# Optimization experiments

Measured on AMD Instinct MI355X. Metric: run time of the kernel, lower is better.

The kernel has to match this reference:

```python
import jax, jax.numpy as jnp
import numpy as np

H = 8  # nhead
EPS = 1e-5


def _ln(x, g, b):
    mu = x.mean(-1, keepdims=True)
    var = ((x - mu) ** 2).mean(-1, keepdims=True)
    return (x - mu) / jnp.sqrt(var + EPS) * g + b


def _mha(q_in, kv_in, w_qkv, b_qkv, w_o, b_o, mask):
    # PyTorch nn.MultiheadAttention with packed in_proj: rows [Wq; Wk; Wv], y = x @ W.T + b
    d = q_in.shape[-1]
    hd = d // H
    wq, wk, wv = jnp.split(w_qkv, 3, axis=0)
    bq, bk, bv = jnp.split(b_qkv, 3)
    B, Lq = q_in.shape[0], q_in.shape[1]
    Lk = kv_in.shape[1]
    q = (q_in @ wq.T + bq).reshape(B, Lq, H, hd).transpose(0, 2, 1, 3)
    k = (kv_in @ wk.T + bk).reshape(B, Lk, H, hd).transpose(0, 2, 1, 3)
    v = (kv_in @ wv.T + bv).reshape(B, Lk, H, hd).transpose(0, 2, 1, 3)
    s = jnp.einsum('bhqd,bhkd->bhqk', q, k) * np.float32(1.0 / np.sqrt(hd))
    if mask is not None:
        s = s + mask  # additive causal mask, (Lq, Lk) broadcast
    a = jax.nn.softmax(s, axis=-1)
    o = jnp.einsum('bhqk,bhkd->bhqd', a, v).transpose(0, 2, 1, 3).reshape(B, Lq, d)
    return o @ w_o.T + b_o


def _forward(z, target_ids, tok_emb, pos_emb, lp_w, lp_b, lp_ln_g, lp_ln_b,
             sa_qkv_w, sa_qkv_b, sa_out_w, sa_out_b,
             ca_qkv_w, ca_qkv_b, ca_out_w, ca_out_b,
             ln1_g, ln1_b, ln2_g, ln2_b, ln3_g, ln3_b,
             ff1_w, ff1_b, ff2_w, ff2_b, op_w, op_b):
    B, L = target_ids.shape
    # latent_proj: Linear -> GELU (exact) -> LayerNorm; (B, 1, d) memory
    mem = jax.nn.gelu(z @ lp_w.T + lp_b, approximate=False)
    mem = _ln(mem, lp_ln_g, lp_ln_b)[:, None, :]
    # token + positional embedding
    x = tok_emb[target_ids] + pos_emb[jnp.arange(L)][None, :, :]
    # causal additive mask (upper triangle = -inf)
    causal = jnp.where(jnp.tril(jnp.ones((L, L), dtype=bool)), 0.0, -1e9).astype(x.dtype)
    n_layers = sa_qkv_w.shape[0]
    for i in range(n_layers):  # post-norm TransformerDecoderLayer (norm_first=False)
        x = _ln(x + _mha(x, x, sa_qkv_w[i], sa_qkv_b[i], sa_out_w[i], sa_out_b[i], causal), ln1_g[i], ln1_b[i])
        x = _ln(x + _mha(x, mem, ca_qkv_w[i], ca_qkv_b[i], ca_out_w[i], ca_out_b[i], None), ln2_g[i], ln2_b[i])
        ff = jax.nn.relu(x @ ff1_w[i].T + ff1_b[i]) @ ff2_w[i].T + ff2_b[i]
        x = _ln(x + ff, ln3_g[i], ln3_b[i])
    return x @ op_w.T + op_b  # (B, L, vocab)


def setup_inputs() -> dict:
    B, L, D, LAT, V, NL = 32, 128, 512, 256, 50257, 4
    DF = 4 * D
    key = jax.random.key(0)
    ks = jax.random.split(key, 20)
    s = 0.02
    n = lambda k, shp: jax.random.normal(k, shp, dtype=jnp.float32) * s
    return {
        'z': jax.random.normal(ks[0], (B, LAT), dtype=jnp.float32),
        'target_ids': jax.random.randint(ks[1], (B, L), 0, V),
        'tok_emb': n(ks[2], (V, D)),
        'pos_emb': n(ks[3], (L, D)),
        'lp_w': n(ks[4], (D, LAT)), 'lp_b': jnp.zeros((D,)),
        'lp_ln_g': jnp.ones((D,)), 'lp_ln_b': jnp.zeros((D,)),
        'sa_qkv_w': n(ks[5], (NL, 3 * D, D)), 'sa_qkv_b': jnp.zeros((NL, 3 * D)),
        'sa_out_w': n(ks[6], (NL, D, D)), 'sa_out_b': jnp.zeros((NL, D)),
        'ca_qkv_w': n(ks[7], (NL, 3 * D, D)), 'ca_qkv_b': jnp.zeros((NL, 3 * D)),
        'ca_out_w': n(ks[8], (NL, D, D)), 'ca_out_b': jnp.zeros((NL, D)),
        'ln1_g': jnp.ones((NL, D)), 'ln1_b': jnp.zeros((NL, D)),
        'ln2_g': jnp.ones((NL, D)), 'ln2_b': jnp.zeros((NL, D)),
        'ln3_g': jnp.ones((NL, D)), 'ln3_b': jnp.zeros((NL, D)),
        'ff1_w': n(ks[9], (NL, DF, D)), 'ff1_b': jnp.zeros((NL, DF)),
        'ff2_w': n(ks[10], (NL, D, DF)), 'ff2_b': jnp.zeros((NL, D)),
        'op_w': n(ks[11], (V, D)), 'op_b': jnp.zeros((V,)),
    }


def reference(z, target_ids, tok_emb, pos_emb, lp_w, lp_b, lp_ln_g, lp_ln_b,
              sa_qkv_w, sa_qkv_b, sa_out_w, sa_out_b,
              ca_qkv_w, ca_qkv_b, ca_out_w, ca_out_b,
              ln1_g, ln1_b, ln2_g, ln2_b, ln3_g, ln3_b,
              ff1_w, ff1_b, ff2_w, ff2_b, op_w, op_b):
    return _forward(z, target_ids, tok_emb, pos_emb, lp_w, lp_b, lp_ln_g, lp_ln_b,
                    sa_qkv_w, sa_qkv_b, sa_out_w, sa_out_b,
                    ca_qkv_w, ca_qkv_b, ca_out_w, ca_out_b,
                    ln1_g, ln1_b, ln2_g, ln2_b, ln3_g, ln3_b,
                    ff1_w, ff1_b, ff2_w, ff2_b, op_w, op_b)
```

## Files before the change

### kernel.cpp

```cpp
#include <hip/hip_runtime.h>
#include <math.h>

typedef __attribute__((ext_vector_type(8))) short short8;
typedef __attribute__((ext_vector_type(4))) float f32x4;
typedef __attribute__((ext_vector_type(4))) float f4;
typedef __attribute__((ext_vector_type(4))) unsigned short us4;
typedef unsigned short u16;

#define Bn 32
#define Ln 128
#define Dn 512
#define LATn 256
#define Vn 50257
#define VPAD 50304
#define DFn 2048
#define Hn 8
#define HDn 64

#define GLD(src, dst) __builtin_amdgcn_global_load_lds( \
    (const __attribute__((address_space(1))) unsigned int*)(src), \
    (__attribute__((address_space(3))) unsigned int*)(dst), 16, 0, 0)

__device__ __forceinline__ u16 f2bf(float f) {
  union { float f; unsigned u; } v; v.f = f;
  unsigned r = 0x7FFFu + ((v.u >> 16) & 1u);
  return (u16)((v.u + r) >> 16);
}
__device__ __forceinline__ float bf2f(u16 u) {
  union { unsigned u; float f; } v; v.u = ((unsigned)u) << 16;
  return v.f;
}

__global__ __launch_bounds__(256)
void k_cvt_all(const float* __restrict__ s0, const float* __restrict__ s1,
               const float* __restrict__ s2, const float* __restrict__ s3,
               const float* __restrict__ s4, us4* __restrict__ dst) {
  const int C0 = 786432;
  const int C1 = 1048576;
  const int C2 = 2097152;
  const int C3 = 3145728;
  const int C4 = 9584640;
  const int OPN4 = 6432896;
  int i = blockIdx.x * blockDim.x + threadIdx.x;
  int stride = gridDim.x * blockDim.x;
  for (; i < C4; i += stride) {
    const f4* src; int off; bool valid = true;
    if (i < C0)      { src = (const f4*)s0; off = i; }
    else if (i < C1) { src = (const f4*)s1; off = i - C0; }
    else if (i < C2) { src = (const f4*)s2; off = i - C1; }
    else if (i < C3) { src = (const f4*)s3; off = i - C2; }
    else             { src = (const f4*)s4; off = i - C3; valid = off < OPN4; }
    us4 o;
    if (valid) {
      f4 v = src[off];
      o[0] = f2bf(v[0]); o[1] = f2bf(v[1]); o[2] = f2bf(v[2]); o[3] = f2bf(v[3]);
    } else { o[0] = 0; o[1] = 0; o[2] = 0; o[3] = 0; }
    dst[i] = o;
  }
}

__global__ __launch_bounds__(256)
void k_latent_mem(const float* __restrict__ z, const float* __restrict__ lp_w,
                  const float* __restrict__ lp_b, const float* __restrict__ g,
                  const float* __restrict__ be, float* __restrict__ mem) {
  __shared__ float zs[LATn];
  __shared__ float red[16];
  int b = blockIdx.x, t = threadIdx.x;
  zs[t] = z[b * LATn + t];
  __syncthreads();
  float h[2];
  #pragma unroll
  for (int j = 0; j < 2; j++) {
    int oj = t + j * 256;
    const float* w = lp_w + (size_t)oj * LATn;
    float s0 = 0, s1 = 0, s2 = 0, s3 = 0;
    for (int k = 0; k < LATn; k += 4) {
      s0 += zs[k] * w[k]; s1 += zs[k+1] * w[k+1];
      s2 += zs[k+2] * w[k+2]; s3 += zs[k+3] * w[k+3];
    }
    float x = s0 + s1 + s2 + s3 + lp_b[oj];
    h[j] = 0.5f * x * (1.0f + erff(x * 0.70710678118654752f));
  }
  float sum = h[0] + h[1], sq = h[0]*h[0] + h[1]*h[1];
  for (int off = 32; off; off >>= 1) {
    sum += __shfl_down(sum, off, 64);
    sq  += __shfl_down(sq,  off, 64);
  }
  int lane = t & 63, wid = t >> 6;
  if (!lane) { red[wid] = sum; red[8 + wid] = sq; }
  __syncthreads();
  float ts = red[0] + red[1] + red[2] + red[3];
  float tq = red[8] + red[9] + red[10] + red[11];
  float mu = ts * (1.0f / Dn);
  float var = tq * (1.0f / Dn) - mu * mu;
  float rstd = rsqrtf(fmaxf(var, 0.0f) + 1e-5f);
  #pragma unroll
  for (int j = 0; j < 2; j++) {
    int oj = t + j * 256;
    mem[b * Dn + oj] = (h[j] - mu) * rstd * g[oj] + be[oj];
  }
}

__global__ __launch_bounds__(256)
void k_ca(const float* __restrict__ mem, const float* __restrict__ ca_qkv_w,
          const float* __restrict__ ca_qkv_b, const float* __restrict__ ca_out_w,
          const float* __restrict__ ca_out_b, float* __restrict__ ca_add) {
  int blk = blockIdx.x;
  int i = blk >> 5, b = blk & 31, t = threadIdx.x;
  __shared__ float ms[Dn];
  __shared__ float vs[Dn];
  ms[t] = mem[b * Dn + t];
  ms[t + 256] = mem[b * Dn + t + 256];
  __syncthreads();
  const float* wv = ca_qkv_w + ((size_t)i * 1536 + 1024) * Dn;
  const float* bv = ca_qkv_b + i * 1536 + 1024;
  for (int j = t; j < Dn; j += 256) {
    const float* w = wv + (size_t)j * Dn;
    float s0 = 0, s1 = 0, s2 = 0, s3 = 0;
    for (int k = 0; k < Dn; k += 4) {
      s0 += ms[k]*w[k]; s1 += ms[k+1]*w[k+1]; s2 += ms[k+2]*w[k+2]; s3 += ms[k+3]*w[k+3];
    }
    vs[j] = s0 + s1 + s2 + s3 + bv[j];
  }
  __syncthreads();
  const float* wo = ca_out_w + (size_t)i * Dn * Dn;
  const float* bo = ca_out_b + i * Dn;
  for (int j = t; j < Dn; j += 256) {
    const float* w = wo + (size_t)j * Dn;
    float s0 = 0, s1 = 0, s2 = 0, s3 = 0;
    for (int k = 0; k < Dn; k += 4) {
      s0 += vs[k]*w[k]; s1 += vs[k+1]*w[k+1]; s2 += vs[k+2]*w[k+2]; s3 += vs[k+3]*w[k+3];
    }
    ca_add[((size_t)i * Bn + b) * Dn + j] = s0 + s1 + s2 + s3 + bo[j];
  }
}

__global__ __launch_bounds__(128)
void k_embed(const int* __restrict__ ids, const float* __restrict__ tok,
             const float* __restrict__ pos, float* __restrict__ X,
             u16* __restrict__ Xb) {
  int r = blockIdx.x;
  int l = r & (Ln - 1);
  int id = ids[r];
  int c = threadIdx.x * 4;
  f4 te = *(const f4*)&tok[(size_t)id * Dn + c];
  f4 pe = *(const f4*)&pos[(size_t)l * Dn + c];
  f4 v = te + pe;
  *(f4*)&X[(size_t)r * Dn + c] = v;
  us4 o = { f2bf(v[0]), f2bf(v[1]), f2bf(v[2]), f2bf(v[3]) };
  *(us4*)&Xb[(size_t)r * Dn + c] = o;
}

__global__ __launch_bounds__(128)
void k_add_ln(float* __restrict__ X, u16* __restrict__ Xb,
              const u16* __restrict__ Y, const float* __restrict__ g,
              const float* __restrict__ be) {
  int r = blockIdx.x, t = threadIdx.x;
  int c = t * 4;
  f4 x = *(const f4*)&X[(size_t)r * Dn + c];
  us4 yb = *(const us4*)&Y[(size_t)r * Dn + c];
  f4 v;
  v[0] = x[0] + bf2f(yb[0]); v[1] = x[1] + bf2f(yb[1]);
  v[2] = x[2] + bf2f(yb[2]); v[3] = x[3] + bf2f(yb[3]);
  float sum = v[0] + v[1] + v[2] + v[3];
  float sq = v[0]*v[0] + v[1]*v[1] + v[2]*v[2] + v[3]*v[3];
  for (int off = 32; off; off >>= 1) {
    sum += __shfl_down(sum, off, 64);
    sq  += __shfl_down(sq,  off, 64);
  }
  __shared__ float red[4];
  int lane = t & 63, w = t >> 6;
  if (!lane) { red[w] = sum; red[2 + w] = sq; }
  __syncthreads();
  sum = red[0] + red[1]; sq = red[2] + red[3];
  float mu = sum * (1.0f / Dn);
  float var = sq * (1.0f / Dn) - mu * mu;
  float rstd = rsqrtf(fmaxf(var, 0.0f) + 1e-5f);
  f4 gg = *(const f4*)&g[c];
  f4 bb = *(const f4*)&be[c];
  f4 o = (v - mu) * rstd * gg + bb;
  *(f4*)&X[(size_t)r * Dn + c] = o;
  us4 ob = { f2bf(o[0]), f2bf(o[1]), f2bf(o[2]), f2bf(o[3]) };
  *(us4*)&Xb[(size_t)r * Dn + c] = ob;
}

__global__ __launch_bounds__(128)
void k_add_ln12(float* __restrict__ X, u16* __restrict__ Xb,
                const u16* __restrict__ Y, const float* __restrict__ CA,
                const float* __restrict__ g1, const float* __restrict__ b1,
                const float* __restrict__ g2, const float* __restrict__ b2) {
  int r = blockIdx.x, t = threadIdx.x;
  int c = t * 4;
  __shared__ float red[8];
  int lane = t & 63, w = t >> 6;
  f4 x = *(const f4*)&X[(size_t)r * Dn + c];
  us4 yb = *(const us4*)&Y[(size_t)r * Dn + c];
  f4 v;
  v[0] = x[0] + bf2f(yb[0]); v[1] = x[1] + bf2f(yb[1]);
  v[2] = x[2] + bf2f(yb[2]); v[3] = x[3] + bf2f(yb[3]);
  float sum = v[0] + v[1] + v[2] + v[3];
  float sq = v[0]*v[0] + v[1]*v[1] + v[2]*v[2] + v[3]*v[3];
  for (int off = 32; off; off >>= 1) {
    sum += __shfl_down(sum, off, 64);
    sq  += __shfl_down(sq,  off, 64);
  }
  if (!lane) { red[w] = sum; red[2 + w] = sq; }
  __syncthreads();
  sum = red[0] + red[1]; sq = red[2] + red[3];
  float mu = sum * (1.0f / Dn);
  float var = sq * (1.0f / Dn) - mu * mu;
  float rstd = rsqrtf(fmaxf(var, 0.0f) + 1e-5f);
  f4 g1v = *(const f4*)&g1[c];
  f4 b1v = *(const f4*)&b1[c];
  f4 o1 = (v - mu) * rstd * g1v + b1v;
  f4 ca = *(const f4*)&CA[(size_t)(r >> 7) * Dn + c];
  f4 v2 = o1 + ca;
  float sum2 = v2[0] + v2[1] + v2[2] + v2[3];
  float sq2 = v2[0]*v2[0] + v2[1]*v2[1] + v2[2]*v2[2] + v2[3]*v2[3];
  for (int off = 32; off; off >>= 1) {
    sum2 += __shfl_down(sum2, off, 64);
    sq2  += __shfl_down(sq2,  off, 64);
  }
  if (!lane) { red[4 + w] = sum2; red[6 + w] = sq2; }
  __syncthreads();
  sum2 = red[4] + red[5]; sq2 = red[6] + red[7];
  float mu2 = sum2 * (1.0f / Dn);
  float var2 = sq2 * (1.0f / Dn) - mu2 * mu2;
  float rstd2 = rsqrtf(fmaxf(var2, 0.0f) + 1e-5f);
  f4 g2v = *(const f4*)&g2[c];
  f4 b2v = *(const f4*)&b2[c];
  f4 o2 = (v2 - mu2) * rstd2 * g2v + b2v;
  *(f4*)&X[(size_t)r * Dn + c] = o2;
  us4 ob = { f2bf(o2[0]), f2bf(o2[1]), f2bf(o2[2]), f2bf(o2[3]) };
  *(us4*)&Xb[(size_t)r * Dn + c] = ob;
}

__global__ __launch_bounds__(256, 1)
void k_attn_m(const u16* __restrict__ QKV, u16* __restrict__ Ob) {
  constexpr int QS = 0;
  constexpr int KS = 9216;
  constexpr int SFB = 36864;
  constexpr int VTB = 36864 + 66048;
  constexpr int MXB = VTB + 17408;
  constexpr int LXB = MXB + 1024;
  __shared__ __align__(16) char smem[LXB + 1024];
  u16* U = (u16*)smem;
  float* Sf = (float*)(smem + SFB);
  u16* Vt = (u16*)(smem + VTB);
  float* Mx = (float*)(smem + MXB);
  float* Lx = (float*)(smem + LXB);

  int bh = blockIdx.x, b = bh >> 3, h = bh & 7;
  int tid = threadIdx.x, lane = tid & 63, wid = tid >> 6;
  int r = tid & 127, half = tid >> 7;

  {
    const u16* qk = QKV + (size_t)(b * 128 + r) * 1536 + (half ? 512 : 0) + h * 64;
    u16* dst = U + (half ? KS : QS) + r * 72;
    #pragma unroll
    for (int i = 0; i < 64; i += 8)
      *(short8*)(dst + i) = *(const short8*)(qk + i);
    const u16* vsrc = QKV + (size_t)(b * 128 + r) * 1536 + 1024 + h * 64 + half * 32;
    #pragma unroll
    for (int i = 0; i < 32; i += 8) {
      short8 v = *(const short8*)(vsrc + i);
      #pragma unroll
      for (int j = 0; j < 8; j++)
        Vt[(half * 32 + i + j) * 136 + r] = (u16)v[j];
    }
  }
  __syncthreads();

  int qb = wid * 32;
  int fr = lane & 15, qk8 = (lane >> 4) * 8, qrl = (lane >> 4) * 4;
  f32x4 sacc[2][8] = {};
  #pragma unroll
  for (int s = 0; s < 2; s++) {
    short8 av[2], bv[8];
    #pragma unroll
    for (int mi = 0; mi < 2; mi++)
      av[mi] = *(const short8*)(U + QS + (qb + mi * 16 + fr) * 72 + s * 32 + qk8);
    #pragma unroll
    for (int nj = 0; nj < 8; nj++)
      bv[nj] = *(const short8*)(U + KS + (nj * 16 + fr) * 72 + s * 32 + qk8);
    #pragma unroll
    for (int mi = 0; mi < 2; mi++)
      #pragma unroll
      for (int nj = 0; nj < 8; nj++)
        sacc[mi][nj] = __builtin_amdgcn_mfma_f32_16x16x32_bf16(
            av[mi], bv[nj], sacc[mi][nj], 0, 0, 0);
  }
  #pragma unroll
  for (int mi = 0; mi < 2; mi++)
    #pragma unroll
    for (int nj = 0; nj < 8; nj++)
      #pragma unroll
      for (int g = 0; g < 4; g++) {
        int q = qb + mi * 16 + qrl + g;
        int k = nj * 16 + fr;
        Sf[q * 129 + k] = (k <= q) ? sacc[mi][nj][g] * 0.125f : -1e30f;
      }
  __syncthreads();

  int kr = half * 64;
  float m = -1e30f;
  for (int k = 0; k < 64; k++) m = fmaxf(m, Sf[r * 129 + kr + k]);
  Mx[half * 128 + r] = m;
  __syncthreads();
  float mm = fmaxf(Mx[r], Mx[128 + r]);
  float l = 0.0f;
  for (int k = 0; k < 64; k++) {
    float p = __expf(Sf[r * 129 + kr + k] - mm);
    Sf[r * 129 + kr + k] = p;
    l += p;
  }
  Lx[half * 128 + r] = l;
  __syncthreads();
  float linv = 1.0f / (Lx[r] + Lx[128 + r]);
  #pragma unroll
  for (int kc = 0; kc < 8; kc++) {
    short8 pv;
    #pragma unroll
    for (int j = 0; j < 8; j++)
      pv[j] = (short)f2bf(Sf[r * 129 + kr + kc * 8 + j] * linv);
    *(short8*)(U + r * 136 + kr + kc * 8) = pv;
  }
  __syncthreads();

  f32x4 oacc[2][4] = {};
  #pragma unroll
  for (int ks = 0; ks < 4; ks++) {
    short8 av[2], bv[4];
    #pragma unroll
    for (int mi = 0; mi < 2; mi++)
      av[mi] = *(const short8*)(U + (qb + mi * 16 + fr) * 136 + ks * 32 + qk8);
    #pragma unroll
    for (int nj = 0; nj < 4; nj++)
      bv[nj] = *(const short8*)(Vt + (nj * 16 + fr) * 136 + ks * 32 + qk8);
    #pragma unroll
    for (int mi = 0; mi < 2; mi++)
      #pragma unroll
      for (int nj = 0; nj < 4; nj++)
        oacc[mi][nj] = __builtin_amdgcn_mfma_f32_16x16x32_bf16(
            av[mi], bv[nj], oacc[mi][nj], 0, 0, 0);
  }
  #pragma unroll
  for (int mi = 0; mi < 2; mi++)
    #pragma unroll
    for (int nj = 0; nj < 4; nj++)
      #pragma unroll
      for (int g = 0; g < 4; g++) {
        int q = qb + mi * 16 + qrl + g;
        int d = nj * 16 + fr;
        Ob[(size_t)(b * 128 + q) * 512 + h * 64 + d] = f2bf(oacc[mi][nj][g]);
      }
}

template <int EPI, int BNT>
__global__ __launch_bounds__(256, (BNT == 128 ? 2 : 3))
void k_gemm_bt(const u16* __restrict__ A, const u16* __restrict__ Bw,
               const float* __restrict__ bias, void* __restrict__ Cout,
               int gm, int N, int K, int ldc) {
  constexpr int NREP = BNT / 32;
  constexpr int ASTRIDE = 128 * 64;
  constexpr int BSTRIDE = BNT * 64;
  constexpr int TSTRIDE = BNT + 4;
  constexpr int NLA = 4;
  constexpr int NLB = BNT / 32;
  __shared__ __align__(16) char smem[(ASTRIDE + BSTRIDE) * 4];
  u16* As = (u16*)smem;
  u16* Bs = (u16*)(smem + ASTRIDE * 4);
  float* Ts = (float*)smem;

  int lin = blockIdx.x;
  int bm = lin % gm, bn = lin / gm;
  int tid = threadIdx.x, lane = tid & 63, wid = tid >> 6;
  int wr = wid >> 1, wc = wid & 1;
  int fr = lane & 15, q = lane >> 4;
  f32x4 acc[4][NREP] = {};

  auto stage = [&](int it) {
    int buf = it & 1;
    #pragma unroll
    for (int l = 0; l < NLA; l++) {
      int c = tid + l * 256;
      int row = c >> 3;
      int kcg = (c & 7) ^ (row & 7);
      GLD(A + (size_t)(bm * 128 + row) * K + it * 64 + kcg * 8,
          (char*)(As + buf * ASTRIDE) + c * 16);
    }
    #pragma unroll
    for (int l = 0; l < NLB; l++) {
      int c = tid + l * 256;
      int row = c >> 3;
      int kcg = (c & 7) ^ (row & 7);
      GLD(Bw + (size_t)(bn * BNT + row) * K + it * 64 + kcg * 8,
          (char*)(Bs + buf * BSTRIDE) + c * 16);
    }
  };

  int nt = K >> 6;
  stage(0);
  for (int it = 0; it < nt; ++it) {
    int cur = it & 1;
    if (it + 1 < nt) {
      stage(it + 1);
      if constexpr (BNT == 128) asm volatile("s_waitcnt vmcnt(8)" ::: "memory");
      else                      asm volatile("s_waitcnt vmcnt(6)" ::: "memory");
    } else {
      asm volatile("s_waitcnt vmcnt(0)" ::: "memory");
    }
    __builtin_amdgcn_sched_barrier(0);
    __builtin_amdgcn_s_barrier();
    __builtin_amdgcn_sched_barrier(0);
    short8 av[2][4], bv[2][NREP];
    #pragma unroll
    for (int s = 0; s < 2; s++) {
      #pragma unroll
      for (int mi = 0; mi < 4; mi++) {
        int row = wr * 64 + mi * 16 + fr;
        int phys = (s * 4 + q) ^ (row & 7);
        av[s][mi] = *(const short8*)&As[cur * ASTRIDE + row * 64 + phys * 8];
      }
      #pragma unroll
      for (int nj = 0; nj < NREP; nj++) {
        int row = wc * (BNT / 2) + nj * 16 + fr;
        int phys = (s * 4 + q) ^ (row & 7);
        bv[s][nj] = *(const short8*)&Bs[cur * BSTRIDE + row * 64 + phys * 8];
      }
    }
    #pragma unroll
    for (int s = 0; s < 2; s++)
      #pragma unroll
      for (int mi = 0; mi < 4; mi++)
        #pragma unroll
        for (int nj = 0; nj < NREP; nj++)
          acc[mi][nj] = __builtin_amdgcn_mfma_f32_16x16x32_bf16(
              av[s][mi], bv[s][nj], acc[mi][nj], 0, 0, 0);
    asm volatile("s_waitcnt lgkmcnt(0)" ::: "memory");
    __builtin_amdgcn_sched_barrier(0);
    __builtin_amdgcn_s_barrier();
    __builtin_amdgcn_sched_barrier(0);
  }

  float bb[NREP];
  #pragma unroll
  for (int nj = 0; nj < NREP; nj++) {
    int cg = bn * BNT + wc * (BNT / 2) + nj * 16 + fr;
    bb[nj] = (cg < N) ? bias[cg] : 0.0f;
  }
  int rl0 = (lane >> 4) * 4;
  #pragma unroll
  for (int mi = 0; mi < 4; mi++) {
    #pragma unroll
    for (int nj = 0; nj < NREP; nj++) {
      int colL = wc * (BNT / 2) + nj * 16 + fr;
      #pragma unroll
      for (int r = 0; r < 4; r++)
        Ts[(wr * 16 + rl0 + r) * TSTRIDE + colL] = acc[mi][nj][r] + bb[nj];
    }
    __syncthreads();
    constexpr int ITERS = (32 * BNT) / 256;
    #pragma unroll
    for (int i = 0; i < ITERS; i++) {
      int flat = i * 256 + tid;
      int rowf = flat / BNT, col = flat % BNT;
      float v = Ts[rowf * TSTRIDE + col];
      int row_g = bm * 128 + (rowf >> 4) * 64 + mi * 16 + (rowf & 15);
      int col_g = bn * BNT + col;
      size_t off = (size_t)row_g * ldc + col_g;
      if (EPI == 0) {
        if (col_g < N) ((float*)Cout)[off] = v;
      } else if (EPI == 1) {
        ((u16*)Cout)[off] = f2bf(fmaxf(v, 0.0f));
      } else {
        ((u16*)Cout)[off] = f2bf(v);
      }
    }
    if (mi < 3) __syncthreads();
  }
}

extern "C" void kernel_launch(void* const* d_in, const int* in_sizes, int n_in,
                              void* d_out, int out_size, void* d_ws, size_t ws_size,
                              hipStream_t stream) {
  const float* z        = (const float*)d_in[0];
  const int*   ids      = (const int*)d_in[1];
  const float* tok      = (const float*)d_in[2];
  const float* pos      = (const float*)d_in[3];
  const float* lp_w     = (const float*)d_in[4];
  const float* lp_b     = (const float*)d_in[5];
  const float* lp_g     = (const float*)d_in[6];
  const float* lp_be    = (const float*)d_in[7];
  const float* sa_qkv_w = (const float*)d_in[8];
  const float* sa_qkv_b = (const float*)d_in[9];
  const float* sa_out_w = (const float*)d_in[10];
  const float* sa_out_b = (const float*)d_in[11];
  const float* ca_qkv_w = (const float*)d_in[12];
  const float* ca_qkv_b = (const float*)d_in[13];
  const float* ca_out_w = (const float*)d_in[14];
  const float* ca_out_b = (const float*)d_in[15];
  const float* ln1_g    = (const float*)d_in[16];
  const float* ln1_b    = (const float*)d_in[17];
  const float* ln2_g    = (const float*)d_in[18];
  const float* ln2_b    = (const float*)d_in[19];
  const float* ln3_g    = (const float*)d_in[20];
  const float* ln3_b    = (const float*)d_in[21];
  const float* ff1_w    = (const float*)d_in[22];
  const float* ff1_b    = (const float*)d_in[23];
  const float* ff2_w    = (const float*)d_in[24];
  const float* ff2_b    = (const float*)d_in[25];
  const float* op_w     = (const float*)d_in[26];
  const float* op_b     = (const float*)d_in[27];

  char* ws = (char*)d_ws;
  float* X      = (float*)(ws + 0);
  u16*   Yb     = (u16*)(ws + 8388608);
  u16*   QKVb   = (u16*)(ws + 16777216);
  u16*   Xb     = (u16*)(ws + 29360128);
  u16*   Ob     = (u16*)(ws + 33554432);
  u16*   H1b    = (u16*)(ws + 37748736);
  float* mem    = (float*)(ws + 54525952);
  float* ca_add = (float*)(ws + 54657024);
  u16*   Wa     = (u16*)(ws + 55050240);

  u16* Wqkv = Wa;
  u16* Wout = Wa + 3145728;
  u16* Wff1 = Wa + 4194304;
  u16* Wff2 = Wa + 8388608;
  u16* Wop  = Wa + 12582912;

  k_latent_mem<<<Bn, 256, 0, stream>>>(z, lp_w, lp_b, lp_g, lp_be, mem);
  k_ca<<<4 * Bn, 256, 0, stream>>>(mem, ca_qkv_w, ca_qkv_b, ca_out_w, ca_out_b, ca_add);
  k_embed<<<Bn * Ln, 128, 0, stream>>>(ids, tok, pos, X, Xb);
  k_cvt_all<<<2048, 256, 0, stream>>>(sa_qkv_w, sa_out_w, ff1_w, ff2_w, op_w,
                                      (us4*)Wa);

  const int M = Bn * Ln;
  for (int i = 0; i < 4; i++) {
    k_gemm_bt<2, 128><<<32 * 12, 256, 0, stream>>>(
        Xb, Wqkv + (size_t)i * 1536 * Dn, sa_qkv_b + i * 1536, QKVb, 32, 1536, Dn, 1536);
    k_attn_m<<<Bn * Hn, 256, 0, stream>>>(QKVb, Ob);
    k_gemm_bt<2, 64><<<32 * 8, 256, 0, stream>>>(
        Ob, Wout + (size_t)i * Dn * Dn, sa_out_b + i * Dn, Yb, 32, Dn, Dn, Dn);
    k_add_ln12<<<M, 128, 0, stream>>>(X, Xb, Yb, ca_add + (size_t)i * Bn * Dn,
                                      ln1_g + i * Dn, ln1_b + i * Dn,
                                      ln2_g + i * Dn, ln2_b + i * Dn);
    k_gemm_bt<1, 128><<<32 * 16, 256, 0, stream>>>(
        Xb, Wff1 + (size_t)i * DFn * Dn, ff1_b + i * DFn, H1b, 32, DFn, Dn, DFn);
    k_gemm_bt<2, 64><<<32 * 8, 256, 0, stream>>>(
        H1b, Wff2 + (size_t)i * Dn * DFn, ff2_b + i * Dn, Yb, 32, Dn, DFn, Dn);
    k_add_ln<<<M, 128, 0, stream>>>(X, Xb, Yb, ln3_g + i * Dn, ln3_b + i * Dn);
  }

  k_gemm_bt<0, 128><<<32 * 393, 256, 0, stream>>>(
      Xb, Wop, op_b, (float*)d_out, 32, Vn, Dn, Vn);
}
```

Measured before the change: 893.6 us.

## Use 256x256 tiled GEMM kernel with 512 threads for vocab projection

Adds a dedicated GEMM kernel for the final output projection using 256x256 block tiles, 8 waves, double-buffered swizzled LDS staging via global_load_lds, and an LDS-staged fp32 epilogue. It replaces the 128-wide tile kernel for this large-N GEMM to raise operand reuse and cut global load traffic per output. It uses 128KB of LDS and many accumulator registers, which limits occupancy to about one block per CU.

New measurement: 819.2 us. -8.3%, faster.

```diff
diff --git a/kernel.cpp b/kernel.cpp
--- a/kernel.cpp
+++ b/kernel.cpp
@@ -478,6 +478,119 @@
       }
     }
     if (mi < 3) __syncthreads();
+  }
+}
+
+__global__ __launch_bounds__(512, 2)
+void k_gemm_v256(const u16* __restrict__ A, const u16* __restrict__ Bw,
+                 const float* __restrict__ bias, float* __restrict__ Cout,
+                 int gm, int N, int K, int ldc) {
+  constexpr int ASTRIDE = 256 * 64;
+  constexpr int BSTRIDE = 256 * 64;
+  constexpr int TSTRIDE = 256 + 4;
+  __shared__ __align__(16) char smem[(ASTRIDE + BSTRIDE) * 4];
+  u16* As = (u16*)smem;
+  u16* Bs = (u16*)(smem + ASTRIDE * 4);
+  float* Ts = (float*)smem;
+
+  int lin = blockIdx.x;
+  int bm = lin % gm, bn = lin / gm;
+  int tid = threadIdx.x, lane = tid & 63, wid = tid >> 6;
+  int wr = wid >> 2, wc = wid & 3;
+  int fr = lane & 15, q = lane >> 4;
+  f32x4 acc[8][4] = {};
+
+  auto stage = [&](int it) {
+    int buf = it & 1;
+    #pragma unroll
+    for (int l = 0; l < 4; l++) {
+      int c = tid + l * 512;
+      int row = c >> 3;
+      int kcg = (c & 7) ^ (row & 7);
+      GLD(A + (size_t)(bm * 256 + row) * K + it * 64 + kcg * 8,
+          (char*)(As + buf * ASTRIDE) + c * 16);
+    }
+    #pragma unroll
+    for (int l = 0; l < 4; l++) {
+      int c = tid + l * 512;
+      int row = c >> 3;
+      int rowg = bn * 256 + row;
+      if (rowg > VPAD - 1) rowg = VPAD - 1;
+      int kcg = (c & 7) ^ (row & 7);
+      GLD(Bw + (size_t)rowg * K + it * 64 + kcg * 8,
+          (char*)(Bs + buf * BSTRIDE) + c * 16);
+    }
+  };
+
+  int nt = K >> 6;
+  stage(0);
+  for (int it = 0; it < nt; ++it) {
+    int cur = it & 1;
+    if (it + 1 < nt) {
+      stage(it + 1);
+      asm volatile("s_waitcnt vmcnt(8)" ::: "memory");
+    } else {
+      asm volatile("s_waitcnt vmcnt(0)" ::: "memory");
+    }
+    __builtin_amdgcn_sched_barrier(0);
+    __builtin_amdgcn_s_barrier();
+    __builtin_amdgcn_sched_barrier(0);
+    #pragma unroll
+    for (int s = 0; s < 2; s++) {
+      short8 av[8], bv[4];
+      #pragma unroll
+      for (int mi = 0; mi < 8; mi++) {
+        int row = wr * 128 + mi * 16 + fr;
+        int phys = (s * 4 + q) ^ (row & 7);
+        av[mi] = *(const short8*)&As[cur * ASTRIDE + row * 64 + phys * 8];
+      }
+      #pragma unroll
+      for (int nj = 0; nj < 4; nj++) {
+        int row = wc * 64 + nj * 16 + fr;
+        int phys = (s * 4 + q) ^ (row & 7);
+        bv[nj] = *(const short8*)&Bs[cur * BSTRIDE + row * 64 + phys * 8];
+      }
+      #pragma unroll
+      for (int mi = 0; mi < 8; mi++)
+        #pragma unroll
+        for (int nj = 0; nj < 4; nj++)
+          acc[mi][nj] = __builtin_amdgcn_mfma_f32_16x16x32_bf16(
+              av[mi], bv[nj], acc[mi][nj], 0, 0, 0);
+    }
+    asm volatile("s_waitcnt lgkmcnt(0)" ::: "memory");
+    __builtin_amdgcn_sched_barrier(0);
+    __builtin_amdgcn_s_barrier();
+    __builtin_amdgcn_sched_barrier(0);
+  }
+
+  float bb[4];
+  #pragma unroll
+  for (int nj = 0; nj < 4; nj++) {
+    int cg = bn * 256 + wc * 64 + nj * 16 + fr;
+    bb[nj] = (cg < N) ? bias[cg] : 0.0f;
+  }
+  int rl0 = (lane >> 4) * 4;
+  #pragma unroll
+  for (int mi = 0; mi < 8; mi++) {
+    #pragma unroll
+    for (int nj = 0; nj < 4; nj++) {
+      int colL = wc * 64 + nj * 16 + fr;
+      #pragma unroll
+      for (int r = 0; r < 4; r++)
+        Ts[(wr * 16 + rl0 + r) * TSTRIDE + colL] = acc[mi][nj][r] + bb[nj];
+    }
+    __syncthreads();
+    #pragma unroll
+    for (int i = 0; i < 16; i++) {
+      int flat = i * 512 + tid;
+      int rowf = flat >> 8, col = flat & 255;
+      float v = Ts[rowf * TSTRIDE + col];
+      int row_g = bm * 256 + (rowf >> 4) * 128 + mi * 16 + (rowf & 15);
+      int col_g = bn * 256 + col;
+      if (col_g < N)
+        Cout[(size_t)row_g * ldc + col_g] = v;
+    }
+    if (mi < 7) __syncthreads();
   }
 }
 
@@ -553,6 +666,6 @@
     k_add_ln<<<M, 128, 0, stream>>>(X, Xb, Yb, ln3_g + i * Dn, ln3_b + i * Dn);
   }
 
-  k_gemm_bt<0, 128><<<32 * 393, 256, 0, stream>>>(
-      Xb, Wop, op_b, (float*)d_out, 32, Vn, Dn, Vn);
-}
+  k_gemm_v256<<<16 * 197, 512, 0, stream>>>(
+      Xb, Wop, op_b, (float*)d_out, 16, Vn, Dn, Vn);
+}
```
